# Performance work log

Hardware: AMD Instinct MI355X
Metric: run time of the kernel (lower is better)

Reference implementation:

```python
import jax, jax.numpy as jnp
import numpy as np

N_NODES = 100000
N_EDGES = 1600000
IN_CH = 64
HID = 64


def setup_inputs() -> dict:
    key = jax.random.key(0)
    ks = jax.random.split(key, 6)
    x = jax.random.normal(ks[0], (N_NODES, IN_CH), dtype=jnp.float32)
    edge_index = jax.random.randint(ks[1], (2, N_EDGES), 0, N_NODES, dtype=jnp.int64)
    # Glorot-ish scaled weights
    W1 = jax.random.normal(ks[2], (IN_CH, HID), dtype=jnp.float32) / np.sqrt(IN_CH)
    b1 = jnp.zeros((HID,), dtype=jnp.float32)
    W2 = jax.random.normal(ks[3], (HID, HID), dtype=jnp.float32) / np.sqrt(HID)
    b2 = jnp.zeros((HID,), dtype=jnp.float32)
    Wl = jax.random.normal(ks[4], (HID, 1), dtype=jnp.float32) / np.sqrt(HID)
    bl = jnp.zeros((1,), dtype=jnp.float32)
    return {"x": x, "edge_index": edge_index, "W1": W1, "b1": b1,
            "W2": W2, "b2": b2, "Wl": Wl, "bl": bl}


def _gcn_conv(h, W, b, src, dst, norm, n_nodes):
    # GCNConv: linear transform, then sym-normalized neighborhood sum, then bias.
    h = h @ W                                  # [N, out]
    msg = h[src] * norm[:, None]               # [E+N, out] gather + scale
    agg = jax.ops.segment_sum(msg, dst, num_segments=n_nodes)  # scatter-add
    return agg + b


def reference(x, edge_index, W1, b1, W2, b2, Wl, bl):
    n = x.shape[0]
    self_loop = jnp.arange(n, dtype=edge_index.dtype)
    src = jnp.concatenate([edge_index[0], self_loop])  # message sources (x_j)
    dst = jnp.concatenate([edge_index[1], self_loop])  # aggregation targets
    # symmetric normalization deg^{-1/2}[src] * deg^{-1/2}[dst], deg incl. self-loops
    deg = jax.ops.segment_sum(jnp.ones_like(dst, dtype=x.dtype), dst, num_segments=n)
    dinv = jnp.where(deg > 0, jax.lax.rsqrt(jnp.maximum(deg, 1.0)), 0.0)
    norm = dinv[src] * dinv[dst]

    h = jax.nn.relu(_gcn_conv(x, W1, b1, src, dst, norm, n))
    # dropout is identity in eval mode
    h = _gcn_conv(h, W2, b2, src, dst, norm, n)
    return jax.nn.sigmoid(h @ Wl + bl)          # [N, 1]
```

## Files before the change

kernel.cpp:

```cpp
#include <hip/hip_runtime.h>
#include <hip/hip_fp16.h>

#define CH 64
#define NBUCK 1024
#define BSHIFT 7
#define BMASK 127
#define NBLK_P 512
#define RPMASK 0x1FFFFFu

typedef _Float16 f16x4 __attribute__((ext_vector_type(4)));
typedef float    f32x4 __attribute__((ext_vector_type(4)));


__global__ __launch_bounds__(256) void k_hist(const int* __restrict__ dst,
                                              int* __restrict__ blkhist, int E) {
    __shared__ int h[NBUCK];
    for (int i = threadIdx.x; i < NBUCK; i += blockDim.x) h[i] = 0;
    __syncthreads();
    int chunk = (E + NBLK_P - 1) / NBLK_P;
    int beg = blockIdx.x * chunk;
    int end = min(beg + chunk, E);
    for (int e = beg + threadIdx.x; e < end; e += blockDim.x)
        atomicAdd(&h[dst[e] >> BSHIFT], 1);
    __syncthreads();
    for (int i = threadIdx.x; i < NBUCK; i += blockDim.x)
        blkhist[blockIdx.x * NBUCK + i] = h[i];
}

__global__ __launch_bounds__(256) void k_bucketscan(const int* __restrict__ blkhist,
                                                    int* __restrict__ off_t,
                                                    int* __restrict__ tot) {
    int lane = threadIdx.x & 63;
    int t = (blockIdx.x * blockDim.x + threadIdx.x) >> 6;
    int v[8], pre[8];
    int sum = 0;
#pragma unroll
    for (int j = 0; j < 8; ++j) {
        v[j] = blkhist[(lane * 8 + j) * NBUCK + t];
        pre[j] = sum;
        sum += v[j];
    }
    int sc = sum;
#pragma unroll
    for (int o = 1; o < 64; o <<= 1) {
        int u = __shfl_up(sc, o, 64);
        if (lane >= o) sc += u;
    }
    int excl = sc - sum;
#pragma unroll
    for (int j = 0; j < 8; ++j)
        off_t[t * NBLK_P + lane * 8 + j] = excl + pre[j];
    if (lane == 63) tot[t] = sc;
}

__global__ __launch_bounds__(1024) void k_scantot(const int* __restrict__ tot,
                                                  int* __restrict__ bbase) {
    __shared__ int sh[NBUCK];
    int t = threadIdx.x;
    int v = tot[t];
    sh[t] = v;
    __syncthreads();
    for (int o = 1; o < NBUCK; o <<= 1) {
        int u = (t >= o) ? sh[t - o] : 0;
        __syncthreads();
        sh[t] += u;
        __syncthreads();
    }
    bbase[t] = sh[t] - v;
    if (t == NBUCK - 1) bbase[NBUCK] = sh[t];
}

__global__ __launch_bounds__(256) void k_partition(const int* __restrict__ src,
                                                   const int* __restrict__ dst,
                                                   const int* __restrict__ off_t,
                                                   const int* __restrict__ bbase,
                                                   unsigned int* __restrict__ ebuf, int E) {
    __shared__ int cur[NBUCK];
    for (int i = threadIdx.x; i < NBUCK; i += blockDim.x)
        cur[i] = bbase[i] + off_t[i * NBLK_P + blockIdx.x];
    __syncthreads();
    int chunk = (E + NBLK_P - 1) / NBLK_P;
    int beg = blockIdx.x * chunk;
    int end = min(beg + chunk, E);
    for (int e = beg + threadIdx.x; e < end; e += blockDim.x) {
        int s = src[e];
        int d = dst[e];
        int p = atomicAdd(&cur[d >> BSHIFT], 1);
        ebuf[p] = ((unsigned int)(d & BMASK) << 17) | (unsigned int)s;
    }
}

__global__ __launch_bounds__(128) void k_bucket_csr(const unsigned int* __restrict__ ebuf,
                                                    const int* __restrict__ bbase,
                                                    int* __restrict__ row_ptr,
                                                    float* __restrict__ dinv,
                                                    int* __restrict__ col, int n) {
    __shared__ int cnt[128];
    __shared__ int cur[128];
    __shared__ int sc[128];
    int t = threadIdx.x;
    int k = blockIdx.x;
    int e0 = bbase[k], e1 = bbase[k + 1];
    cnt[t] = 0;
    __syncthreads();
    for (int e = e0 + t; e < e1; e += 128)
        atomicAdd(&cnt[ebuf[e] >> 17], 1);
    __syncthreads();
    int c = cnt[t];
    sc[t] = c;
    __syncthreads();
    for (int o = 1; o < 128; o <<= 1) {
        int v = (t >= o) ? sc[t - o] : 0;
        __syncthreads();
        sc[t] += v;
        __syncthreads();
    }
    int excl = sc[t] - c;
    int prow = e0 + excl;
    int node = (k << BSHIFT) + t;
    if (node < n) {
        row_ptr[node] = prow | (c << 21);
        dinv[node] = rsqrtf((float)(c + 1));
    }
    cur[t] = prow;
    __syncthreads();
    for (int e = e0 + t; e < e1; e += 128) {
        unsigned int u = ebuf[e];
        int p = atomicAdd(&cur[u >> 17], 1);
        col[p] = (int)(u & 0x1FFFFu);
    }
}


__global__ __launch_bounds__(256) void k_init(const float* __restrict__ W2,
                                              const float* __restrict__ Wl,
                                              float* __restrict__ wt,
                                              const float* __restrict__ W1,
                                              __half* __restrict__ wfrag) {
    if (threadIdx.x < 64) {
        int k = threadIdx.x;
        float s = 0.0f;
#pragma unroll 8
        for (int c = 0; c < CH; ++c) s = fmaf(W2[k * CH + c], Wl[c], s);
        wt[k] = s;
    }
    for (int idx = threadIdx.x; idx < 1024; idx += 256) {
        int f = idx >> 6;
        int l = idx & 63;
        int w4 = f >> 2, t = f & 3;
        int kb = w4 * 16 + 4 * (l >> 4);
        int c  = t * 16 + (l & 15);
#pragma unroll
        for (int b = 0; b < 4; ++b) {
            float wv = W1[(kb + b) * CH + c];
            __half hi = __float2half(wv);
            float lo = wv - __half2float(hi);
            wfrag[(size_t)f * 256 + l * 4 + b] = hi;
            wfrag[4096 + (size_t)f * 256 + l * 4 + b] = __float2half(lo);
        }
    }
}


__global__ __launch_bounds__(256) void k_gemm_mfma(const float* __restrict__ in,
                                                   const __half* __restrict__ wfrag,
                                                   const float* __restrict__ dinv,
                                                   __half* __restrict__ hs, int n) {
    if (blockIdx.x == 0 && threadIdx.x < CH)
        hs[(size_t)n * CH + threadIdx.x] = __float2half(0.0f);

    int lane = threadIdx.x & 63;
    int wid  = (blockIdx.x * blockDim.x + threadIdx.x) >> 6;
    int nw   = (gridDim.x * blockDim.x) >> 6;

    const f16x4* wf = (const f16x4*)wfrag;
    f16x4 wh[16], wl[16];
#pragma unroll
    for (int f = 0; f < 16; ++f) {
        wh[f] = wf[f * 64 + lane];
        wl[f] = wf[1024 + f * 64 + lane];
    }

    int r15 = lane & 15;
    int q   = lane >> 4;
    int ngrp = (n + 15) >> 4;

    for (int g = wid; g < ngrp; g += nw) {
        int base = g << 4;
        int arow = min(base + r15, n - 1);
        const float* ap = in + (size_t)arow * CH + 4 * q;

        f32x4 acc0 = {0.f, 0.f, 0.f, 0.f};
        f32x4 acc1 = {0.f, 0.f, 0.f, 0.f};
        f32x4 acc2 = {0.f, 0.f, 0.f, 0.f};
        f32x4 acc3 = {0.f, 0.f, 0.f, 0.f};

#pragma unroll
        for (int w4 = 0; w4 < 4; ++w4) {
            float4 xv = *(const float4*)(ap + w4 * 16);
            f16x4 ah, al;
            ah[0] = (_Float16)xv.x; al[0] = (_Float16)(xv.x - (float)ah[0]);
            ah[1] = (_Float16)xv.y; al[1] = (_Float16)(xv.y - (float)ah[1]);
            ah[2] = (_Float16)xv.z; al[2] = (_Float16)(xv.z - (float)ah[2]);
            ah[3] = (_Float16)xv.w; al[3] = (_Float16)(xv.w - (float)ah[3]);

            acc0 = __builtin_amdgcn_mfma_f32_16x16x16f16(ah, wh[w4 * 4 + 0], acc0, 0, 0, 0);
            acc1 = __builtin_amdgcn_mfma_f32_16x16x16f16(ah, wh[w4 * 4 + 1], acc1, 0, 0, 0);
            acc2 = __builtin_amdgcn_mfma_f32_16x16x16f16(ah, wh[w4 * 4 + 2], acc2, 0, 0, 0);
            acc3 = __builtin_amdgcn_mfma_f32_16x16x16f16(ah, wh[w4 * 4 + 3], acc3, 0, 0, 0);
            acc0 = __builtin_amdgcn_mfma_f32_16x16x16f16(al, wh[w4 * 4 + 0], acc0, 0, 0, 0);
            acc1 = __builtin_amdgcn_mfma_f32_16x16x16f16(al, wh[w4 * 4 + 1], acc1, 0, 0, 0);
            acc2 = __builtin_amdgcn_mfma_f32_16x16x16f16(al, wh[w4 * 4 + 2], acc2, 0, 0, 0);
            acc3 = __builtin_amdgcn_mfma_f32_16x16x16f16(al, wh[w4 * 4 + 3], acc3, 0, 0, 0);
            acc0 = __builtin_amdgcn_mfma_f32_16x16x16f16(ah, wl[w4 * 4 + 0], acc0, 0, 0, 0);
            acc1 = __builtin_amdgcn_mfma_f32_16x16x16f16(ah, wl[w4 * 4 + 1], acc1, 0, 0, 0);
            acc2 = __builtin_amdgcn_mfma_f32_16x16x16f16(ah, wl[w4 * 4 + 2], acc2, 0, 0, 0);
            acc3 = __builtin_amdgcn_mfma_f32_16x16x16f16(ah, wl[w4 * 4 + 3], acc3, 0, 0, 0);
        }

#pragma unroll
        for (int b = 0; b < 4; ++b) {
            int row = base + 4 * q + b;
            if (row < n) {
                float d = dinv[row];
                size_t o = (size_t)row * CH + r15;
                hs[o +  0] = __float2half(acc0[b] * d);
                hs[o + 16] = __float2half(acc1[b] * d);
                hs[o + 32] = __float2half(acc2[b] * d);
                hs[o + 48] = __float2half(acc3[b] * d);
            }
        }
    }
}


__global__ __launch_bounds__(256) void k_gather_gemm(const int* __restrict__ row_ptr,
                                                     const int* __restrict__ col,
                                                     const __half2* __restrict__ hs2,
                                                     const float* __restrict__ dinv,
                                                     const float* __restrict__ wt,
                                                     const float* __restrict__ bias,
                                                     float* __restrict__ z, int n) {
    int lane = threadIdx.x & 63;
    int l    = lane & 31;
    int g    = lane >> 5;
    int wid  = (blockIdx.x * blockDim.x + threadIdx.x) >> 6;
    int nw   = (gridDim.x * blockDim.x) >> 6;

    float2 wt2 = ((const float2*)wt)[l];
    float2 bi2 = ((const float2*)bias)[l];

    int npairs = (n + 1) >> 1;
    int pr = wid;
    if (pr >= npairs) return;

    unsigned pkA = (unsigned)row_ptr[pr << 1];
    unsigned pkB = (unsigned)row_ptr[min((pr << 1) + 1, n - 1)];
    int cv = col[(int)((g ? pkB : pkA) & RPMASK) + l];

    for (; pr < npairs; pr += nw) {
        int a = pr << 1;
        bool hasB = (a + 1) < n;
        int begS = (int)((g ? pkB : pkA) & RPMASK);
        int degS = (int)((g ? pkB : pkA) >> 21);
        int degA = (int)(pkA >> 21), degB = (int)(pkB >> 21);
        int selfS = g ? (hasB ? a + 1 : a) : a;
        int mycv = cv;
        float dA = dinv[a];
        float dB = dinv[hasB ? a + 1 : a];

        __half2 h[32];
#pragma unroll
        for (int r = 0; r < 32; ++r) {
            int cr = __shfl(mycv, r, 32);
            int idx = (r < degS) ? cr : n;
            h[r] = hs2[(size_t)idx * 32 + l];
        }
        __half2 hself = hs2[(size_t)selfS * 32 + l];

        int nxt = pr + nw;
        if (nxt < npairs) {
            int a1 = nxt << 1;
            pkA = (unsigned)row_ptr[a1];
            pkB = (unsigned)row_ptr[min(a1 + 1, n - 1)];
            cv = col[(int)((g ? pkB : pkA) & RPMASK) + l];
        }

        float ax0, ay0, ax1 = 0.f, ay1 = 0.f;
        float ax2 = 0.f, ay2 = 0.f, ax3 = 0.f, ay3 = 0.f;
        {
            float2 fs = __half22float2(hself);
            ax0 = fs.x; ay0 = fs.y;
        }
#pragma unroll
        for (int r = 0; r < 32; r += 4) {
            float2 f0 = __half22float2(h[r]);
            float2 f1 = __half22float2(h[r + 1]);
            float2 f2 = __half22float2(h[r + 2]);
            float2 f3 = __half22float2(h[r + 3]);
            ax0 += f0.x; ay0 += f0.y;
            ax1 += f1.x; ay1 += f1.y;
            ax2 += f2.x; ay2 += f2.y;
            ax3 += f3.x; ay3 += f3.y;
        }
        float accx = (ax0 + ax1) + (ax2 + ax3);
        float accy = (ay0 + ay1) + (ay2 + ay3);

        if (max(degA, degB) > 32) {
            for (int r = 32; r < degS; ++r) {
                float2 f = __half22float2(hs2[(size_t)col[begS + r] * 32 + l]);
                accx += f.x; accy += f.y;
            }
        }

        float d = g ? dB : dA;
        float vx = fmaxf(fmaf(accx, d, bi2.x), 0.0f);
        float vy = fmaxf(fmaf(accy, d, bi2.y), 0.0f);
        float p = fmaf(vx, wt2.x, vy * wt2.y);
#pragma unroll
        for (int o = 16; o > 0; o >>= 1) p += __shfl_xor(p, o, 64);
        p *= d;
        if (l == 0 && (g == 0 || hasB)) z[a + g] = p;
    }
}


__global__ __launch_bounds__(256) void k_head(const int* __restrict__ row_ptr,
                                              const int* __restrict__ col,
                                              const float* __restrict__ z,
                                              const float* __restrict__ dinv,
                                              const float* __restrict__ b2,
                                              const float* __restrict__ Wl,
                                              const float* __restrict__ bl,
                                              float* __restrict__ out, int n) {
    int lane = threadIdx.x & 63;
    float c0 = b2[lane] * Wl[lane];
#pragma unroll
    for (int o = 32; o > 0; o >>= 1) c0 += __shfl_xor(c0, o, 64);
    c0 += bl[0];

    int tid = blockIdx.x * blockDim.x + threadIdx.x;
    int st  = gridDim.x * blockDim.x;
    for (int node = tid; node < n; node += st) {
        unsigned pk = (unsigned)row_ptr[node];
        int beg = (int)(pk & RPMASK);
        int deg = (int)(pk >> 21);
        float s = z[node];
        int e = 0;
        for (; e + 4 <= deg; e += 4) {
            float t0 = z[col[beg + e]];
            float t1 = z[col[beg + e + 1]];
            float t2 = z[col[beg + e + 2]];
            float t3 = z[col[beg + e + 3]];
            s += t0; s += t1; s += t2; s += t3;
        }
        for (; e < deg; ++e) s += z[col[beg + e]];
        float v = dinv[node] * s + c0;
        out[node] = 1.0f / (1.0f + expf(-v));
    }
}


extern "C" void kernel_launch(void* const* d_in, const int* in_sizes, int n_in,
                              void* d_out, int out_size, void* d_ws, size_t ws_size,
                              hipStream_t stream) {
    const float* x   = (const float*)d_in[0];
    const int*   ei  = (const int*)d_in[1];
    const float* W1  = (const float*)d_in[2];
    const float* b1  = (const float*)d_in[3];
    const float* W2  = (const float*)d_in[4];
    const float* b2  = (const float*)d_in[5];
    const float* Wl  = (const float*)d_in[6];
    const float* bl  = (const float*)d_in[7];
    float*       out = (float*)d_out;

    const int N = in_sizes[0] / CH;
    const int E = in_sizes[1] / 2;
    const int* src = ei;
    const int* dst = ei + E;

    const size_t Npad = ((size_t)N + 511) & ~(size_t)511;
    const size_t Epad = ((size_t)E + 511) & ~(size_t)511;
    const size_t COLSZ = Epad + 512;

    float* z        = (float*)d_ws;
    float* dinv     = z + Npad;
    int*   row_ptr  = (int*)(dinv + Npad);
    float* wt       = (float*)(row_ptr + Npad);
    __half* wfrag   = (__half*)(wt + 512);
    int*   col      = (int*)(wfrag + 8192);
    unsigned int* ebuf = (unsigned int*)(col + COLSZ);
    int*   blkhist  = (int*)(ebuf + Epad);
    int*   off_t    = blkhist + (size_t)NBLK_P * NBUCK;
    int*   bbase    = off_t + (size_t)NBLK_P * NBUCK;
    int*   tot      = bbase + NBUCK + 64;
    __half* A       = (__half*)ebuf;

    const int TB = 256;
    const int GRID = 2048;
    const int NB_USED = (N + BMASK) >> BSHIFT;

    k_init<<<1, TB, 0, stream>>>(W2, Wl, wt, W1, wfrag);

    k_hist<<<NBLK_P, TB, 0, stream>>>(dst, blkhist, E);
    k_bucketscan<<<NBUCK * 64 / TB, TB, 0, stream>>>(blkhist, off_t, tot);
    k_scantot<<<1, NBUCK, 0, stream>>>(tot, bbase);
    k_partition<<<NBLK_P, TB, 0, stream>>>(src, dst, off_t, bbase, ebuf, E);
    k_bucket_csr<<<NB_USED, 128, 0, stream>>>(ebuf, bbase, row_ptr, dinv, col, N);

    k_gemm_mfma<<<784, TB, 0, stream>>>(x, wfrag, dinv, A, N);

    k_gather_gemm<<<2 * GRID, TB, 0, stream>>>(row_ptr, col, (const __half2*)A, dinv,
                                               wt, b1, z, N);

    k_head<<<(N + TB - 1) / TB, TB, 0, stream>>>(row_ptr, col, z, dinv, b2, Wl, bl, out, N);
}
```

Before: 196.5 us.

## Replace bucketed two-pass CSR build with atomic degree count and scatter

Swaps the bucket histogram/partition/per-bucket CSR construction for a direct global-atomic degree count, a three-stage prefix scan, and an atomic scatter of source indices into col. Degree zeroing moves into a widened init kernel. The head kernel now uses four lanes per node with a shuffle reduction instead of one thread per node. This cuts kernel count and the intermediate edge buffer pass, but uses global atomics on 100k counters, which can contend, and gives a nondeterministic neighbor order within rows.

```diff
diff --git a/kernel.cpp b/kernel.cpp
--- a/kernel.cpp
+++ b/kernel.cpp
@@ -2,162 +2,114 @@
 #include <hip/hip_fp16.h>
 
 #define CH 64
-#define NBUCK 1024
-#define BSHIFT 7
-#define BMASK 127
-#define NBLK_P 512
 #define RPMASK 0x1FFFFFu
 
 typedef _Float16 f16x4 __attribute__((ext_vector_type(4)));
 typedef float    f32x4 __attribute__((ext_vector_type(4)));
 
 
-__global__ __launch_bounds__(256) void k_hist(const int* __restrict__ dst,
-                                              int* __restrict__ blkhist, int E) {
-    __shared__ int h[NBUCK];
-    for (int i = threadIdx.x; i < NBUCK; i += blockDim.x) h[i] = 0;
-    __syncthreads();
-    int chunk = (E + NBLK_P - 1) / NBLK_P;
-    int beg = blockIdx.x * chunk;
-    int end = min(beg + chunk, E);
-    for (int e = beg + threadIdx.x; e < end; e += blockDim.x)
-        atomicAdd(&h[dst[e] >> BSHIFT], 1);
-    __syncthreads();
-    for (int i = threadIdx.x; i < NBUCK; i += blockDim.x)
-        blkhist[blockIdx.x * NBUCK + i] = h[i];
-}
-
-__global__ __launch_bounds__(256) void k_bucketscan(const int* __restrict__ blkhist,
-                                                    int* __restrict__ off_t,
-                                                    int* __restrict__ tot) {
-    int lane = threadIdx.x & 63;
-    int t = (blockIdx.x * blockDim.x + threadIdx.x) >> 6;
-    int v[8], pre[8];
-    int sum = 0;
-#pragma unroll
-    for (int j = 0; j < 8; ++j) {
-        v[j] = blkhist[(lane * 8 + j) * NBUCK + t];
-        pre[j] = sum;
-        sum += v[j];
-    }
-    int sc = sum;
-#pragma unroll
-    for (int o = 1; o < 64; o <<= 1) {
-        int u = __shfl_up(sc, o, 64);
-        if (lane >= o) sc += u;
-    }
-    int excl = sc - sum;
-#pragma unroll
-    for (int j = 0; j < 8; ++j)
-        off_t[t * NBLK_P + lane * 8 + j] = excl + pre[j];
-    if (lane == 63) tot[t] = sc;
-}
-
-__global__ __launch_bounds__(1024) void k_scantot(const int* __restrict__ tot,
-                                                  int* __restrict__ bbase) {
-    __shared__ int sh[NBUCK];
+__global__ __launch_bounds__(256) void k_init(const float* __restrict__ W2,
+                                              const float* __restrict__ Wl,
+                                              float* __restrict__ wt,
+                                              const float* __restrict__ W1,
+                                              __half* __restrict__ wfrag,
+                                              int* __restrict__ deg, int nsc) {
+    int tid = blockIdx.x * blockDim.x + threadIdx.x;
+    for (int i = tid; i < nsc; i += gridDim.x * blockDim.x) deg[i] = 0;
+    if (blockIdx.x == 0) {
+        if (threadIdx.x < 64) {
+            int k = threadIdx.x;
+            float s = 0.0f;
+#pragma unroll 8
+            for (int c = 0; c < CH; ++c) s = fmaf(W2[k * CH + c], Wl[c], s);
+            wt[k] = s;
+        }
+        for (int idx = threadIdx.x; idx < 1024; idx += 256) {
+            int f = idx >> 6;
+            int l = idx & 63;
+            int w4 = f >> 2, t = f & 3;
+            int kb = w4 * 16 + 4 * (l >> 4);
+            int c  = t * 16 + (l & 15);
+#pragma unroll
+            for (int b = 0; b < 4; ++b) {
+                float wv = W1[(kb + b) * CH + c];
+                __half hi = __float2half(wv);
+                float lo = wv - __half2float(hi);
+                wfrag[(size_t)f * 256 + l * 4 + b] = hi;
+                wfrag[4096 + (size_t)f * 256 + l * 4 + b] = __float2half(lo);
+            }
+        }
+    }
+}
+
+
+__global__ __launch_bounds__(256) void k_deg(const int* __restrict__ dst,
+                                             int* __restrict__ deg, int E) {
+    int tid = blockIdx.x * blockDim.x + threadIdx.x;
+    int st  = gridDim.x * blockDim.x;
+    for (int e = tid; e < E; e += st)
+        atomicAdd(&deg[dst[e]], 1);
+}
+
+__global__ __launch_bounds__(1024) void k_scan1(const int* __restrict__ deg,
+                                                int* __restrict__ escan,
+                                                int* __restrict__ bsum) {
+    __shared__ int sh[1024];
     int t = threadIdx.x;
-    int v = tot[t];
+    int i = blockIdx.x * 1024 + t;
+    int v = deg[i];
     sh[t] = v;
     __syncthreads();
-    for (int o = 1; o < NBUCK; o <<= 1) {
+    for (int o = 1; o < 1024; o <<= 1) {
         int u = (t >= o) ? sh[t - o] : 0;
         __syncthreads();
         sh[t] += u;
         __syncthreads();
     }
-    bbase[t] = sh[t] - v;
-    if (t == NBUCK - 1) bbase[NBUCK] = sh[t];
-}
-
-__global__ __launch_bounds__(256) void k_partition(const int* __restrict__ src,
-                                                   const int* __restrict__ dst,
-                                                   const int* __restrict__ off_t,
-                                                   const int* __restrict__ bbase,
-                                                   unsigned int* __restrict__ ebuf, int E) {
-    __shared__ int cur[NBUCK];
-    for (int i = threadIdx.x; i < NBUCK; i += blockDim.x)
-        cur[i] = bbase[i] + off_t[i * NBLK_P + blockIdx.x];
+    escan[i] = sh[t] - v;
+    if (t == 1023) bsum[blockIdx.x] = sh[t];
+}
+
+__global__ __launch_bounds__(1024) void k_scan2(int* __restrict__ bsum, int nb) {
+    __shared__ int sh[1024];
+    int t = threadIdx.x;
+    int v = (t < nb) ? bsum[t] : 0;
+    sh[t] = v;
     __syncthreads();
-    int chunk = (E + NBLK_P - 1) / NBLK_P;
-    int beg = blockIdx.x * chunk;
-    int end = min(beg + chunk, E);
-    for (int e = beg + threadIdx.x; e < end; e += blockDim.x) {
-        int s = src[e];
-        int d = dst[e];
-        int p = atomicAdd(&cur[d >> BSHIFT], 1);
-        ebuf[p] = ((unsigned int)(d & BMASK) << 17) | (unsigned int)s;
-    }
-}
-
-__global__ __launch_bounds__(128) void k_bucket_csr(const unsigned int* __restrict__ ebuf,
-                                                    const int* __restrict__ bbase,
-                                                    int* __restrict__ row_ptr,
-                                                    float* __restrict__ dinv,
-                                                    int* __restrict__ col, int n) {
-    __shared__ int cnt[128];
-    __shared__ int cur[128];
-    __shared__ int sc[128];
-    int t = threadIdx.x;
-    int k = blockIdx.x;
-    int e0 = bbase[k], e1 = bbase[k + 1];
-    cnt[t] = 0;
-    __syncthreads();
-    for (int e = e0 + t; e < e1; e += 128)
-        atomicAdd(&cnt[ebuf[e] >> 17], 1);
-    __syncthreads();
-    int c = cnt[t];
-    sc[t] = c;
-    __syncthreads();
-    for (int o = 1; o < 128; o <<= 1) {
-        int v = (t >= o) ? sc[t - o] : 0;
+    for (int o = 1; o < 1024; o <<= 1) {
+        int u = (t >= o) ? sh[t - o] : 0;
         __syncthreads();
-        sc[t] += v;
+        sh[t] += u;
         __syncthreads();
     }
-    int excl = sc[t] - c;
-    int prow = e0 + excl;
-    int node = (k << BSHIFT) + t;
-    if (node < n) {
-        row_ptr[node] = prow | (c << 21);
-        dinv[node] = rsqrtf((float)(c + 1));
-    }
-    cur[t] = prow;
-    __syncthreads();
-    for (int e = e0 + t; e < e1; e += 128) {
-        unsigned int u = ebuf[e];
-        int p = atomicAdd(&cur[u >> 17], 1);
-        col[p] = (int)(u & 0x1FFFFu);
-    }
-}
-
-
-__global__ __launch_bounds__(256) void k_init(const float* __restrict__ W2,
-                                              const float* __restrict__ Wl,
-                                              float* __restrict__ wt,
-                                              const float* __restrict__ W1,
-                                              __half* __restrict__ wfrag) {
-    if (threadIdx.x < 64) {
-        int k = threadIdx.x;
-        float s = 0.0f;
-#pragma unroll 8
-        for (int c = 0; c < CH; ++c) s = fmaf(W2[k * CH + c], Wl[c], s);
-        wt[k] = s;
-    }
-    for (int idx = threadIdx.x; idx < 1024; idx += 256) {
-        int f = idx >> 6;
-        int l = idx & 63;
-        int w4 = f >> 2, t = f & 3;
-        int kb = w4 * 16 + 4 * (l >> 4);
-        int c  = t * 16 + (l & 15);
-#pragma unroll
-        for (int b = 0; b < 4; ++b) {
-            float wv = W1[(kb + b) * CH + c];
-            __half hi = __float2half(wv);
-            float lo = wv - __half2float(hi);
-            wfrag[(size_t)f * 256 + l * 4 + b] = hi;
-            wfrag[4096 + (size_t)f * 256 + l * 4 + b] = __float2half(lo);
-        }
+    if (t < nb) bsum[t] = sh[t] - v;
+}
+
+__global__ __launch_bounds__(256) void k_scan3(const int* __restrict__ deg,
+                                               const int* __restrict__ escan,
+                                               const int* __restrict__ bsum,
+                                               int* __restrict__ row_ptr,
+                                               int* __restrict__ cur,
+                                               float* __restrict__ dinv, int n) {
+    int i = blockIdx.x * blockDim.x + threadIdx.x;
+    if (i < n) {
+        int d = deg[i];
+        int s = escan[i] + bsum[i >> 10];
+        row_ptr[i] = s | (d << 21);
+        cur[i] = s;
+        dinv[i] = rsqrtf((float)(d + 1));
+    }
+}
+
+__global__ __launch_bounds__(256) void k_scatter(const int* __restrict__ src,
+                                                 const int* __restrict__ dst,
+                                                 int* __restrict__ cur,
+                                                 int* __restrict__ col, int E) {
+    int tid = blockIdx.x * blockDim.x + threadIdx.x;
+    int st  = gridDim.x * blockDim.x;
+    for (int e = tid; e < E; e += st) {
+        int p = atomicAdd(&cur[dst[e]], 1);
+        col[p] = src[e];
     }
 }
 
@@ -341,22 +293,28 @@
 
     int tid = blockIdx.x * blockDim.x + threadIdx.x;
     int st  = gridDim.x * blockDim.x;
-    for (int node = tid; node < n; node += st) {
+    int n4  = n << 2;
+    for (int q = tid; q < n4; q += st) {
+        int node = q >> 2;
+        int sub  = q & 3;
         unsigned pk = (unsigned)row_ptr[node];
         int beg = (int)(pk & RPMASK);
         int deg = (int)(pk >> 21);
-        float s = z[node];
-        int e = 0;
-        for (; e + 4 <= deg; e += 4) {
-            float t0 = z[col[beg + e]];
-            float t1 = z[col[beg + e + 1]];
-            float t2 = z[col[beg + e + 2]];
-            float t3 = z[col[beg + e + 3]];
-            s += t0; s += t1; s += t2; s += t3;
-        }
-        for (; e < deg; ++e) s += z[col[beg + e]];
-        float v = dinv[node] * s + c0;
-        out[node] = 1.0f / (1.0f + expf(-v));
+        float s0 = (sub == 0) ? z[node] : 0.0f;
+        float s1 = 0.0f;
+        int e = sub;
+        for (; e + 4 < deg; e += 8) {
+            s0 += z[col[beg + e]];
+            s1 += z[col[beg + e + 4]];
+        }
+        if (e < deg) s0 += z[col[beg + e]];
+        float s = s0 + s1;
+        s += __shfl_xor(s, 1, 64);
+        s += __shfl_xor(s, 2, 64);
+        if (sub == 0) {
+            float v = dinv[node] * s + c0;
+            out[node] = 1.0f / (1.0f + expf(-v));
+        }
     }
 }
 
@@ -381,6 +339,8 @@
 
     const size_t Npad = ((size_t)N + 511) & ~(size_t)511;
     const size_t Epad = ((size_t)E + 511) & ~(size_t)511;
+    const int    NSC  = (N + 1023) & ~1023;
+    const int    NB1  = NSC >> 10;
     const size_t COLSZ = Epad + 512;
 
     float* z        = (float*)d_ws;
@@ -389,29 +349,28 @@
     float* wt       = (float*)(row_ptr + Npad);
     __half* wfrag   = (__half*)(wt + 512);
     int*   col      = (int*)(wfrag + 8192);
-    unsigned int* ebuf = (unsigned int*)(col + COLSZ);
-    int*   blkhist  = (int*)(ebuf + Epad);
-    int*   off_t    = blkhist + (size_t)NBLK_P * NBUCK;
-    int*   bbase    = off_t + (size_t)NBLK_P * NBUCK;
-    int*   tot      = bbase + NBUCK + 64;
-    __half* A       = (__half*)ebuf;
+    int*   deg      = col + COLSZ;
+    int*   escan    = deg + NSC;
+    int*   cur      = escan + NSC;
+    int*   bsum     = cur + Npad;
+    __half* A       = (__half*)(bsum + 1024);
 
     const int TB = 256;
     const int GRID = 2048;
-    const int NB_USED = (N + BMASK) >> BSHIFT;
-
-    k_init<<<1, TB, 0, stream>>>(W2, Wl, wt, W1, wfrag);
-
-    k_hist<<<NBLK_P, TB, 0, stream>>>(dst, blkhist, E);
-    k_bucketscan<<<NBUCK * 64 / TB, TB, 0, stream>>>(blkhist, off_t, tot);
-    k_scantot<<<1, NBUCK, 0, stream>>>(tot, bbase);
-    k_partition<<<NBLK_P, TB, 0, stream>>>(src, dst, off_t, bbase, ebuf, E);
-    k_bucket_csr<<<NB_USED, 128, 0, stream>>>(ebuf, bbase, row_ptr, dinv, col, N);
+
+    k_init<<<128, TB, 0, stream>>>(W2, Wl, wt, W1, wfrag, deg, NSC);
+
+    k_deg<<<GRID, TB, 0, stream>>>(dst, deg, E);
+    k_scan1<<<NB1, 1024, 0, stream>>>(deg, escan, bsum);
+    k_scan2<<<1, 1024, 0, stream>>>(bsum, NB1);
+    k_scan3<<<(N + TB - 1) / TB, TB, 0, stream>>>(deg, escan, bsum, row_ptr, cur, dinv, N);
+    k_scatter<<<GRID, TB, 0, stream>>>(src, dst, cur, col, E);
 
     k_gemm_mfma<<<784, TB, 0, stream>>>(x, wfrag, dinv, A, N);
 
     k_gather_gemm<<<2 * GRID, TB, 0, stream>>>(row_ptr, col, (const __half2*)A, dinv,
                                                wt, b1, z, N);
 
-    k_head<<<(N + TB - 1) / TB, TB, 0, stream>>>(row_ptr, col, z, dinv, b2, Wl, bl, out, N);
-}
+    k_head<<<((N << 2) + TB - 1) / TB, TB, 0, stream>>>(row_ptr, col, z, dinv,
+                                                        b2, Wl, bl, out, N);
+}
```

New measurement: 346.4 us. +76.3%, slower.
